# Optimization experiments

Measured on AMD Instinct MI355X. Metric: run time of the kernel, lower is better.

The kernel has to match this reference:

```python
import jax, jax.numpy as jnp
import numpy as np

NUM_AGENTS = 64
IN_FEATURES = 512
OUT_FEATURES = 512
BATCH = 2048


def setup_inputs() -> dict:
    key = jax.random.key(0)
    k1, k2, k3, k4 = jax.random.split(key, 4)
    which_agents = jax.random.randint(k1, (BATCH,), 0, NUM_AGENTS, dtype=jnp.int64 if jax.config.jax_enable_x64 else jnp.int32)
    x = jax.random.normal(k2, (BATCH, IN_FEATURES), dtype=jnp.float32)
    # kaiming_uniform_(a=sqrt(5)) -> bound = sqrt(6 / ((1 + 5) * fan_in)) = 1/sqrt(fan_in)
    bound_w = 1.0 / np.sqrt(IN_FEATURES)
    weight = jax.random.uniform(k3, (NUM_AGENTS, OUT_FEATURES, IN_FEATURES), jnp.float32, -bound_w, bound_w)
    bound_b = 1.0 / np.sqrt(IN_FEATURES)
    bias = jax.random.uniform(k4, (NUM_AGENTS, OUT_FEATURES), jnp.float32, -bound_b, bound_b)
    return {"which_agents": which_agents, "input": x, "weight": weight, "bias": bias}


def reference(which_agents, input, weight, bias):
    # weight[which_agents]: [B, out, in]; batched matvec with input [B, in]
    w = weight[which_agents]          # [B, O, I]
    b = bias[which_agents]            # [B, O]
    return jnp.einsum('boi,bi->bo', w, input) + b
```

## Files before the change

kernel.cpp:

```cpp
#include <hip/hip_runtime.h>


constexpr int BATCH  = 2048;
constexpr int NAGENT = 64;
constexpr int IN_F   = 512;
constexpr int OUT_F  = 512;

constexpr int BN  = 128;
constexpr int MCH = 64;
constexpr int XS  = IN_F + 8;

typedef __attribute__((ext_vector_type(8))) short short8;
typedef __attribute__((ext_vector_type(4))) float f32x4;
typedef __attribute__((ext_vector_type(4))) unsigned int u32x4;

__device__ inline unsigned rnd_bf(float f) {
  unsigned u = __float_as_uint(f);
  return u + 0x7FFFu + ((u >> 16) & 1u);
}
__device__ inline unsigned pk_bf(float lo, float hi) {
  return (rnd_bf(lo) >> 16) | (rnd_bf(hi) & 0xFFFF0000u);
}

__global__ __launch_bounds__(1024, 4) void agent_linear_mfma2(
    const int*   __restrict__ which,
    const float* __restrict__ x,
    const float* __restrict__ weight,
    const float* __restrict__ bias,
    float*       __restrict__ out) {
  const int tid   = threadIdx.x;
  const int lane  = tid & 63;
  const int wid   = tid >> 6;
  const int w8    = wid & 7;
  const int kh    = wid >> 3;
  const int agent = blockIdx.y;
  const int obase = blockIdx.x * BN;

  __shared__ int rowlist_s[BATCH];
  __shared__ int wsum_s[16];
  __shared__ __align__(16) unsigned short Xs[MCH * XS];
  __shared__ float Rs[8][MCH][17];

  int2 v = ((const int2*)which)[tid];
  int lc = (v.x == agent) + (v.y == agent);
  int s = lc;
#pragma unroll
  for (int off = 1; off < 64; off <<= 1) {
    int t = __shfl_up(s, off);
    if (lane >= off) s += t;
  }
  if (lane == 63) wsum_s[wid] = s;
  __syncthreads();
  int base = 0, count = 0;
#pragma unroll
  for (int w = 0; w < 16; ++w) {
    int ws = wsum_s[w];
    if (w < wid) base += ws;
    count += ws;
  }
  {
    int pos = base + s - lc;
    if (v.x == agent) rowlist_s[pos++] = 2 * tid;
    if (v.y == agent) rowlist_s[pos]   = 2 * tid + 1;
  }

  const int nl = lane & 15;
  const int kq = lane >> 4;

  const float* wp = weight + ((size_t)(agent * OUT_F + obase + w8 * 16 + nl)) * IN_F
                  + kh * 256 + kq * 8;
  const float  bv = bias[agent * OUT_F + obase + w8 * 16 + nl];

  for (int m0 = 0; m0 < count; m0 += MCH) {
    const int mcount = min(MCH, count - m0);
    __syncthreads();

#pragma unroll
    for (int t = 0; t < 8; ++t) {
      int idx = t * 1024 + tid;
      int r   = idx >> 7;
      int c4  = idx & 127;
      uint2 w2 = {0u, 0u};
      if (r < mcount) {
        float4 xv = *(const float4*)(x + (size_t)rowlist_s[m0 + r] * IN_F + c4 * 4);
        w2.x = pk_bf(xv.x, xv.y);
        w2.y = pk_bf(xv.z, xv.w);
      }
      *(uint2*)&Xs[r * XS + c4 * 4] = w2;
    }
    __syncthreads();

    f32x4 acc[4] = {{0.f,0.f,0.f,0.f},{0.f,0.f,0.f,0.f},
                    {0.f,0.f,0.f,0.f},{0.f,0.f,0.f,0.f}};
    const int kbase = kh * 256;
    float4 pa[2], pb[2];
    pa[0] = *(const float4*)(wp);      pb[0] = *(const float4*)(wp + 4);
    pa[1] = *(const float4*)(wp + 32); pb[1] = *(const float4*)(wp + 36);
#pragma unroll
    for (int k = 0; k < 8; ++k) {
      float4 c0 = pa[k & 1], c1 = pb[k & 1];
      if (k + 2 < 8) {
        pa[k & 1] = *(const float4*)(wp + (k + 2) * 32);
        pb[k & 1] = *(const float4*)(wp + (k + 2) * 32 + 4);
      }
      u32x4 q;
      q[0] = pk_bf(c0.x, c0.y); q[1] = pk_bf(c0.z, c0.w);
      q[2] = pk_bf(c1.x, c1.y); q[3] = pk_bf(c1.z, c1.w);
      short8 bf = __builtin_bit_cast(short8, q);
#pragma unroll
      for (int i = 0; i < 4; ++i) {
        short8 af = *(const short8*)&Xs[(i * 16 + nl) * XS + kbase + k * 32 + kq * 8];
        acc[i] = __builtin_amdgcn_mfma_f32_16x16x32_bf16(af, bf, acc[i], 0, 0, 0);
      }
    }

    if (kh == 1) {
#pragma unroll
      for (int i = 0; i < 4; ++i)
#pragma unroll
        for (int r = 0; r < 4; ++r)
          Rs[w8][i * 16 + kq * 4 + r][nl] = acc[i][r];
    }
    __syncthreads();

    if (kh == 0) {
#pragma unroll
      for (int i = 0; i < 4; ++i) {
#pragma unroll
        for (int r = 0; r < 4; ++r) {
          int m = i * 16 + kq * 4 + r;
          if (m < mcount) {
            out[(size_t)rowlist_s[m0 + m] * OUT_F + obase + w8 * 16 + nl] =
                acc[i][r] + Rs[w8][m][nl] + bv;
          }
        }
      }
    }
  }
}

extern "C" void kernel_launch(void* const* d_in, const int* in_sizes, int n_in,
                              void* d_out, int out_size, void* d_ws, size_t ws_size,
                              hipStream_t stream) {
  const int*   which = (const int*)d_in[0];
  const float* x     = (const float*)d_in[1];
  const float* w     = (const float*)d_in[2];
  const float* b     = (const float*)d_in[3];
  float*       out   = (float*)d_out;

  dim3 grid(OUT_F / BN, NAGENT);
  agent_linear_mfma2<<<grid, dim3(1024), 0, stream>>>(which, x, w, b, out);
}
```

Measured before the change: 107.7 us.

## Prefetch weights before row compaction, remap block order, skip empty MFMA fragments

Weight fragments are now loaded at kernel start, before the agent row-list scan, so their global latency overlaps the compaction. The prefetch depth grows from two to three k-steps and is refilled early for the next M chunk. The grid becomes 1D with an agent/obase swizzle, which changes block-to-XCD placement. MFMA fragments past the valid row count are skipped, zero-filling of padded X rows is dropped, and float-to-bf16 packing uses native __bf16 conversions. The costs are higher register pressure and a skipped-fragment path that depends on never reading the stale padded rows.

After: 104.4 us, median of 2. 1.03x faster.

```diff
diff --git a/kernel.cpp b/kernel.cpp
--- a/kernel.cpp
+++ b/kernel.cpp
@@ -13,16 +13,16 @@
 typedef __attribute__((ext_vector_type(8))) short short8;
 typedef __attribute__((ext_vector_type(4))) float f32x4;
 typedef __attribute__((ext_vector_type(4))) unsigned int u32x4;
+typedef __bf16 bf16x2 __attribute__((ext_vector_type(2)));
 
-__device__ inline unsigned rnd_bf(float f) {
-  unsigned u = __float_as_uint(f);
-  return u + 0x7FFFu + ((u >> 16) & 1u);
-}
 __device__ inline unsigned pk_bf(float lo, float hi) {
-  return (rnd_bf(lo) >> 16) | (rnd_bf(hi) & 0xFFFF0000u);
+  bf16x2 v;
+  v[0] = (__bf16)lo;
+  v[1] = (__bf16)hi;
+  return __builtin_bit_cast(unsigned, v);
 }
 
-__global__ __launch_bounds__(1024, 4) void agent_linear_mfma2(
+__global__ __launch_bounds__(1024, 4) void agent_linear_mfma4(
     const int*   __restrict__ which,
     const float* __restrict__ x,
     const float* __restrict__ weight,
@@ -33,13 +33,30 @@
   const int wid   = tid >> 6;
   const int w8    = wid & 7;
   const int kh    = wid >> 3;
-  const int agent = blockIdx.y;
-  const int obase = blockIdx.x * BN;
+
+  const int bid   = blockIdx.x;
+  const int agent = (bid & 7) | ((bid >> 5) << 3);
+  const int obase = ((bid >> 3) & 3) * BN;
 
   __shared__ int rowlist_s[BATCH];
   __shared__ int wsum_s[16];
   __shared__ __align__(16) unsigned short Xs[MCH * XS];
   __shared__ float Rs[8][MCH][17];
+
+  const int nl = lane & 15;
+  const int kq = lane >> 4;
+
+  const float* wp = weight + ((size_t)(agent * OUT_F + obase + w8 * 16 + nl)) * IN_F
+                  + kh * 256 + kq * 8;
+
+  float4 pa[3], pb[3];
+#pragma unroll
+  for (int j = 0; j < 3; ++j) {
+    pa[j] = *(const float4*)(wp + j * 32);
+    pb[j] = *(const float4*)(wp + j * 32 + 4);
+  }
+
+  const float bv = bias[agent * OUT_F + obase + w8 * 16 + nl];
 
   int2 v = ((const int2*)which)[tid];
   int lc = (v.x == agent) + (v.y == agent);
@@ -63,77 +80,81 @@
     if (v.x == agent) rowlist_s[pos++] = 2 * tid;
     if (v.y == agent) rowlist_s[pos]   = 2 * tid + 1;
   }
-
-  const int nl = lane & 15;
-  const int kq = lane >> 4;
-
-  const float* wp = weight + ((size_t)(agent * OUT_F + obase + w8 * 16 + nl)) * IN_F
-                  + kh * 256 + kq * 8;
-  const float  bv = bias[agent * OUT_F + obase + w8 * 16 + nl];
+  __syncthreads();
 
   for (int m0 = 0; m0 < count; m0 += MCH) {
     const int mcount = min(MCH, count - m0);
-    __syncthreads();
+    const int nfrag  = (mcount + 15) >> 4;
 
 #pragma unroll
     for (int t = 0; t < 8; ++t) {
       int idx = t * 1024 + tid;
       int r   = idx >> 7;
       int c4  = idx & 127;
-      uint2 w2 = {0u, 0u};
       if (r < mcount) {
         float4 xv = *(const float4*)(x + (size_t)rowlist_s[m0 + r] * IN_F + c4 * 4);
+        uint2 w2;
         w2.x = pk_bf(xv.x, xv.y);
         w2.y = pk_bf(xv.z, xv.w);
+        *(uint2*)&Xs[r * XS + c4 * 4] = w2;
       }
-      *(uint2*)&Xs[r * XS + c4 * 4] = w2;
     }
     __syncthreads();
 
     f32x4 acc[4] = {{0.f,0.f,0.f,0.f},{0.f,0.f,0.f,0.f},
                     {0.f,0.f,0.f,0.f},{0.f,0.f,0.f,0.f}};
     const int kbase = kh * 256;
-    float4 pa[2], pb[2];
-    pa[0] = *(const float4*)(wp);      pb[0] = *(const float4*)(wp + 4);
-    pa[1] = *(const float4*)(wp + 32); pb[1] = *(const float4*)(wp + 36);
 #pragma unroll
     for (int k = 0; k < 8; ++k) {
-      float4 c0 = pa[k & 1], c1 = pb[k & 1];
-      if (k + 2 < 8) {
-        pa[k & 1] = *(const float4*)(wp + (k + 2) * 32);
-        pb[k & 1] = *(const float4*)(wp + (k + 2) * 32 + 4);
+      float4 c0 = pa[k % 3], c1 = pb[k % 3];
+      if (k + 3 < 8) {
+        pa[k % 3] = *(const float4*)(wp + (k + 3) * 32);
+        pb[k % 3] = *(const float4*)(wp + (k + 3) * 32 + 4);
       }
       u32x4 q;
       q[0] = pk_bf(c0.x, c0.y); q[1] = pk_bf(c0.z, c0.w);
       q[2] = pk_bf(c1.x, c1.y); q[3] = pk_bf(c1.z, c1.w);
-      short8 bf = __builtin_bit_cast(short8, q);
+      short8 bfr = __builtin_bit_cast(short8, q);
 #pragma unroll
       for (int i = 0; i < 4; ++i) {
-        short8 af = *(const short8*)&Xs[(i * 16 + nl) * XS + kbase + k * 32 + kq * 8];
-        acc[i] = __builtin_amdgcn_mfma_f32_16x16x32_bf16(af, bf, acc[i], 0, 0, 0);
+        if (i < nfrag) {
+          short8 af = *(const short8*)&Xs[(i * 16 + nl) * XS + kbase + k * 32 + kq * 8];
+          acc[i] = __builtin_amdgcn_mfma_f32_16x16x32_bf16(af, bfr, acc[i], 0, 0, 0);
+        }
       }
     }
 
     if (kh == 1) {
 #pragma unroll
       for (int i = 0; i < 4; ++i)
+        if (i < nfrag)
 #pragma unroll
-        for (int r = 0; r < 4; ++r)
-          Rs[w8][i * 16 + kq * 4 + r][nl] = acc[i][r];
+          for (int r = 0; r < 4; ++r)
+            Rs[w8][i * 16 + kq * 4 + r][nl] = acc[i][r];
     }
     __syncthreads();
 
     if (kh == 0) {
 #pragma unroll
       for (int i = 0; i < 4; ++i) {
+        if (i < nfrag) {
 #pragma unroll
-        for (int r = 0; r < 4; ++r) {
-          int m = i * 16 + kq * 4 + r;
-          if (m < mcount) {
-            out[(size_t)rowlist_s[m0 + m] * OUT_F + obase + w8 * 16 + nl] =
-                acc[i][r] + Rs[w8][m][nl] + bv;
+          for (int r = 0; r < 4; ++r) {
+            int m = i * 16 + kq * 4 + r;
+            if (m < mcount) {
+              out[(size_t)rowlist_s[m0 + m] * OUT_F + obase + w8 * 16 + nl] =
+                  acc[i][r] + Rs[w8][m][nl] + bv;
+            }
           }
         }
+      }
+    }
+
+    if (m0 + MCH < count) {
+#pragma unroll
+      for (int j = 0; j < 3; ++j) {
+        pa[j] = *(const float4*)(wp + j * 32);
+        pb[j] = *(const float4*)(wp + j * 32 + 4);
       }
     }
   }
@@ -148,6 +169,6 @@
   const float* b     = (const float*)d_in[3];
   float*       out   = (float*)d_out;
 
-  dim3 grid(OUT_F / BN, NAGENT);
-  agent_linear_mfma2<<<grid, dim3(1024), 0, stream>>>(which, x, w, b, out);
+  dim3 grid(OUT_F / BN * NAGENT);
+  agent_linear_mfma4<<<grid, dim3(1024), 0, stream>>>(which, x, w, b, out);
 }
```
